# Performance work log

Measured on AMD Instinct MI355X. Metric: run time of the kernel, lower is better.

Reference implementation:

```python
import jax, jax.numpy as jnp
import numpy as np
import math

B, Q, K = 2, 2048, 2048
C_Q = C_K = C_V = 256
H, D = 8, 32  # no_heads, c_hidden


def setup_inputs() -> dict:
    key = jax.random.key(0)
    ks = jax.random.split(key, 9)
    s_in = 1.0 / math.sqrt(C_Q)
    return {
        "q_x": jax.random.normal(ks[0], (B, Q, C_Q), jnp.float32),
        "kv_x": jax.random.normal(ks[1], (B, K, C_K), jnp.float32),
        "bias": jax.random.normal(ks[2], (B, 1, Q, K), jnp.float32),
        # projection weights, stored torch-style as [out, in]
        "Wq": jax.random.normal(ks[3], (H * D, C_Q), jnp.float32) * s_in,
        "Wk": jax.random.normal(ks[4], (H * D, C_K), jnp.float32) * s_in,
        "Wv": jax.random.normal(ks[5], (H * D, C_V), jnp.float32) * s_in,
        "Wo": jax.random.normal(ks[6], (C_Q, H * D), jnp.float32) * (1.0 / math.sqrt(H * D)),
        "bo": jnp.zeros((C_Q,), jnp.float32),
        "Wg": jax.random.normal(ks[7], (H * D, C_Q), jnp.float32) * 0.02,
        "bg": jnp.ones((H * D,), jnp.float32),
    }


def reference(q_x, kv_x, bias, Wq, Wk, Wv, Wo, bo, Wg, bg):
    inv_sqrt_d = 1.0 / math.sqrt(D)
    # project and split heads: [B, S, H, D]
    q = (q_x @ Wq.T).reshape(B, Q, H, D) * inv_sqrt_d
    k = (kv_x @ Wk.T).reshape(B, K, H, D)
    v = (kv_x @ Wv.T).reshape(B, K, H, D)
    # scores [B, H, Q, K] with broadcast bias
    a = jnp.einsum("bqhd,bkhd->bhqk", q, k) + bias
    a = jax.nn.softmax(a, axis=-1)
    # attend: [B, Q, H, D]
    o = jnp.einsum("bhqk,bkhd->bqhd", a, v)
    # output gating from query data
    g = jax.nn.sigmoid(q_x @ Wg.T + bg).reshape(B, Q, H, D)
    o = o * g
    o = o.reshape(B, Q, H * D)
    return o @ Wo.T + bo
```

## Files before the change

### kernel.cpp

```cpp
#include <hip/hip_runtime.h>
#include <hip/hip_bf16.h>

#define B_ 2
#define SEQ 2048
#define CIN 256
#define H_ 8
#define D_ 32

typedef __attribute__((ext_vector_type(4))) short short4v;
typedef __attribute__((ext_vector_type(8))) short short8v;
typedef __attribute__((ext_vector_type(4))) float floatx4;

static __device__ __forceinline__ unsigned short f2bf(float f) {
  union { float f; unsigned u; } v; v.f = f;
  unsigned r = v.u + 0x7fff + ((v.u >> 16) & 1);
  return (unsigned short)(r >> 16);
}
static __device__ __forceinline__ float bf2f(unsigned short h) {
  union { unsigned u; float f; } v; v.u = ((unsigned)h) << 16; return v.f;
}

__global__ __launch_bounds__(256) void prep_w(const float* wq, const float* wk,
                                              const float* wv, const float* wg,
                                              const float* wo, unsigned short* o) {
  int i = blockIdx.x * 256 + threadIdx.x;
  int m = i >> 16, j = i & 65535;
  const float* s = (m == 0) ? wq : (m == 1) ? wk : (m == 2) ? wv : (m == 3) ? wg : wo;
  o[i] = f2bf(s[j]);
}

#define PK_STRIDE 72
__global__ __launch_bounds__(256) void proj_kernel(
    const float* qx, const float* kvx, const unsigned short* wbf,
    unsigned short* qp, unsigned short* kp, unsigned short* vt,
    unsigned short* gate, const float* bg,
    const unsigned short* ao, float* outp, const float* bo, int mode_base) {
  __shared__ unsigned short xs[32 * PK_STRIDE];
  __shared__ unsigned short wsld[256 * PK_STRIDE];
  const int mode = mode_base + blockIdx.y;
  const int tid = threadIdx.x;
  const int lane = tid & 63;
  const int wid = tid >> 6;
  const int m0 = blockIdx.x * 32;
  const int g = lane >> 4, l15 = lane & 15;

  const int wsel_idx = (mode == 0) ? 0 : (mode == 1) ? 3 : (mode == 2) ? 1 : (mode == 3) ? 2 : 4;
  const unsigned short* wsel = wbf + wsel_idx * 65536;

  floatx4 acc[2][4];
#pragma unroll
  for (int mt = 0; mt < 2; ++mt)
#pragma unroll
    for (int nt = 0; nt < 4; ++nt) {
      floatx4 z = {0.f, 0.f, 0.f, 0.f};
      acc[mt][nt] = z;
    }

  for (int k0 = 0; k0 < 256; k0 += 64) {
    if (mode < 4) {
      const float* X = (mode < 2) ? qx : kvx;
#pragma unroll
      for (int i = 0; i < 8; ++i) {
        int e = tid + i * 256;
        int row = e >> 6, col = e & 63;
        xs[row * PK_STRIDE + col] = f2bf(X[(m0 + row) * 256 + k0 + col]);
      }
    } else {
      int row = tid >> 3, col8 = tid & 7;
      *(short8v*)(xs + row * PK_STRIDE + col8 * 8) =
          *(const short8v*)(ao + (m0 + row) * 256 + k0 + col8 * 8);
    }
#pragma unroll
    for (int i = 0; i < 8; ++i) {
      int c = tid + i * 256;
      int n = c >> 3, col8 = c & 7;
      *(short8v*)(wsld + n * PK_STRIDE + col8 * 8) =
          *(const short8v*)(wsel + n * 256 + k0 + col8 * 8);
    }
    __syncthreads();

#pragma unroll
    for (int ks = 0; ks < 2; ++ks) {
      short8v a[2], bfr[4];
#pragma unroll
      for (int mt = 0; mt < 2; ++mt) {
        const unsigned short* p = xs + (mt * 16 + l15) * PK_STRIDE + ks * 32 + 4 * g;
        short4v lo = *(const short4v*)p;
        short4v hi = *(const short4v*)(p + 16);
        a[mt] = __builtin_shufflevector(lo, hi, 0, 1, 2, 3, 4, 5, 6, 7);
      }
#pragma unroll
      for (int nt = 0; nt < 4; ++nt) {
        int n = wid * 64 + nt * 16 + l15;
        const unsigned short* p = wsld + n * PK_STRIDE + ks * 32 + 4 * g;
        short4v lo = *(const short4v*)p;
        short4v hi = *(const short4v*)(p + 16);
        bfr[nt] = __builtin_shufflevector(lo, hi, 0, 1, 2, 3, 4, 5, 6, 7);
      }
#pragma unroll
      for (int mt = 0; mt < 2; ++mt)
#pragma unroll
        for (int nt = 0; nt < 4; ++nt)
          acc[mt][nt] = __builtin_amdgcn_mfma_f32_16x16x32_bf16(a[mt], bfr[nt], acc[mt][nt], 0, 0, 0);
    }
    __syncthreads();
  }

#pragma unroll
  for (int mt = 0; mt < 2; ++mt) {
#pragma unroll
    for (int nt = 0; nt < 4; ++nt) {
      int n = wid * 64 + nt * 16 + l15;
#pragma unroll
      for (int r = 0; r < 4; ++r) {
        int m = m0 + mt * 16 + 4 * g + r;
        float val = acc[mt][nt][r];
        int b = m >> 11, s = m & 2047;
        if (mode == 0) {
          qp[((b * H_ + (n >> 5)) * SEQ + s) * D_ + (n & 31)] = f2bf(val * 0.17677669529663687f);
        } else if (mode == 1) {
          float sg = 1.f / (1.f + __expf(-(val + bg[n])));
          gate[(b * SEQ + s) * 256 + n] = f2bf(sg);
        } else if (mode == 2) {
          kp[((b * H_ + (n >> 5)) * SEQ + s) * D_ + (n & 31)] = f2bf(val);
        } else if (mode == 3) {
          vt[((b * H_ + (n >> 5)) * D_ + (n & 31)) * SEQ + s] = f2bf(val);
        } else {
          outp[m * 256 + n] = val + bo[n];
        }
      }
    }
  }
}

#define KSTEP 32
#define KLDS_STRIDE 40
#define VLDS_STRIDE 40
#define BIAS_STRIDE 34
__global__ __launch_bounds__(512) void attn_kernel(
    const unsigned short* qp, const unsigned short* kp, const unsigned short* vt,
    const unsigned short* gate, const float* bias, unsigned short* ao) {
  __shared__ unsigned short Ks[H_ * KSTEP * KLDS_STRIDE];
  __shared__ unsigned short Vs[H_ * D_ * VLDS_STRIDE];
  __shared__ float Bs[16 * BIAS_STRIDE];
  const int tid = threadIdx.x;
  const int lane = tid & 63;
  const int h = tid >> 6;
  const int b = blockIdx.y;
  const int q0 = blockIdx.x * 16;
  const int g = lane >> 4, l15 = lane & 15;

  const unsigned short* qpb = qp + ((b * H_ + h) * SEQ + q0 + l15) * D_;
  short4v qlo = *(const short4v*)(qpb + 4 * g);
  short4v qhi = *(const short4v*)(qpb + 16 + 4 * g);
  short8v qfrag = __builtin_shufflevector(qlo, qhi, 0, 1, 2, 3, 4, 5, 6, 7);

  const unsigned short* kpb = kp + (b * H_ + h) * SEQ * D_;
  const unsigned short* vtb = vt + (b * H_ + h) * D_ * SEQ;
  unsigned short* Ksh = Ks + h * KSTEP * KLDS_STRIDE;
  unsigned short* Vsh = Vs + h * D_ * VLDS_STRIDE;

  floatx4 oacc[2];
  {
    floatx4 z = {0.f, 0.f, 0.f, 0.f};
    oacc[0] = z; oacc[1] = z;
  }
  float mrun = -1e30f, lrun = 0.f;

  for (int k0 = 0; k0 < SEQ; k0 += KSTEP) {
#pragma unroll
    for (int c = 0; c < 2; ++c) {
      int f = c * 64 + lane;
      int row = f >> 2, col8 = f & 3;
      *(short8v*)(Ksh + row * KLDS_STRIDE + col8 * 8) =
          *(const short8v*)(kpb + (k0 + row) * D_ + col8 * 8);
    }
#pragma unroll
    for (int c = 0; c < 2; ++c) {
      int f = c * 64 + lane;
      int d = f >> 2, col8 = f & 3;
      *(short8v*)(Vsh + d * VLDS_STRIDE + col8 * 8) =
          *(const short8v*)(vtb + d * SEQ + k0 + col8 * 8);
    }
    {
      int row = tid >> 5, col = tid & 31;
      Bs[row * BIAS_STRIDE + col] = bias[(b * SEQ + q0 + row) * SEQ + k0 + col];
    }
    __syncthreads();

    floatx4 s[2];
#pragma unroll
    for (int kt = 0; kt < 2; ++kt) {
      const unsigned short* p = Ksh + (kt * 16 + l15) * KLDS_STRIDE + 4 * g;
      short4v lo = *(const short4v*)p;
      short4v hi = *(const short4v*)(p + 16);
      short8v kf = __builtin_shufflevector(lo, hi, 0, 1, 2, 3, 4, 5, 6, 7);
      floatx4 z = {0.f, 0.f, 0.f, 0.f};
      s[kt] = __builtin_amdgcn_mfma_f32_16x16x32_bf16(kf, qfrag, z, 0, 0, 0);
    }
    float tmax = -1e30f;
#pragma unroll
    for (int kt = 0; kt < 2; ++kt)
#pragma unroll
      for (int r = 0; r < 4; ++r) {
        float v = s[kt][r] + Bs[l15 * BIAS_STRIDE + kt * 16 + 4 * g + r];
        s[kt][r] = v;
        tmax = fmaxf(tmax, v);
      }
    tmax = fmaxf(tmax, __shfl_xor(tmax, 16, 64));
    tmax = fmaxf(tmax, __shfl_xor(tmax, 32, 64));
    float mnew = fmaxf(mrun, tmax);
    float cs = __expf(mrun - mnew);
    float tsum = 0.f;
    short8v pf;
#pragma unroll
    for (int kt = 0; kt < 2; ++kt)
#pragma unroll
      for (int r = 0; r < 4; ++r) {
        float pv = __expf(s[kt][r] - mnew);
        tsum += pv;
        pf[kt * 4 + r] = (short)f2bf(pv);
      }
    tsum += __shfl_xor(tsum, 16, 64);
    tsum += __shfl_xor(tsum, 32, 64);
    lrun = lrun * cs + tsum;
    mrun = mnew;
    oacc[0] *= cs;
    oacc[1] *= cs;
#pragma unroll
    for (int dt = 0; dt < 2; ++dt) {
      const unsigned short* p = Vsh + (dt * 16 + l15) * VLDS_STRIDE + 4 * g;
      short4v lo = *(const short4v*)p;
      short4v hi = *(const short4v*)(p + 16);
      short8v vf = __builtin_shufflevector(lo, hi, 0, 1, 2, 3, 4, 5, 6, 7);
      oacc[dt] = __builtin_amdgcn_mfma_f32_16x16x32_bf16(vf, pf, oacc[dt], 0, 0, 0);
    }
    __syncthreads();
  }

  float inv_l = 1.f / lrun;
  int q = q0 + l15;
  const unsigned short* gb = gate + ((b * SEQ + q) * 256 + h * D_);
  unsigned short* aob = ao + ((b * SEQ + q) * 256 + h * D_);
#pragma unroll
  for (int dt = 0; dt < 2; ++dt) {
    short4v gv = *(const short4v*)(gb + dt * 16 + 4 * g);
    short4v ov;
#pragma unroll
    for (int r = 0; r < 4; ++r) {
      float o = oacc[dt][r] * inv_l * bf2f((unsigned short)gv[r]);
      ov[r] = (short)f2bf(o);
    }
    *(short4v*)(aob + dt * 16 + 4 * g) = ov;
  }
}

extern "C" void kernel_launch(void* const* d_in, const int* in_sizes, int n_in,
                              void* d_out, int out_size, void* d_ws, size_t ws_size,
                              hipStream_t stream) {
  const float* qx = (const float*)d_in[0];
  const float* kvx = (const float*)d_in[1];
  const float* bias = (const float*)d_in[2];
  const float* Wq = (const float*)d_in[3];
  const float* Wk = (const float*)d_in[4];
  const float* Wv = (const float*)d_in[5];
  const float* Wo = (const float*)d_in[6];
  const float* bo = (const float*)d_in[7];
  const float* Wg = (const float*)d_in[8];
  const float* bg = (const float*)d_in[9];
  float* out = (float*)d_out;

  unsigned short* ws = (unsigned short*)d_ws;
  unsigned short* wbf = ws;
  unsigned short* qp = ws + 327680;
  unsigned short* kp = qp + 1048576;
  unsigned short* vt = kp + 1048576;
  unsigned short* gate = vt + 1048576;
  unsigned short* ao = gate + 1048576;

  prep_w<<<dim3(1280), dim3(256), 0, stream>>>(Wq, Wk, Wv, Wg, Wo, wbf);
  proj_kernel<<<dim3(128, 4), dim3(256), 0, stream>>>(qx, kvx, wbf, qp, kp, vt, gate, bg,
                                                      ao, out, bo, 0);
  attn_kernel<<<dim3(128, 2), dim3(512), 0, stream>>>(qp, kp, vt, gate, bias, ao);
  proj_kernel<<<dim3(128, 1), dim3(256), 0, stream>>>(qx, kvx, wbf, qp, kp, vt, gate, bg,
                                                      ao, out, bo, 4);
}
```

Baseline: 211.4 us.

## Drop LDS staging and online-max softmax; permute head-dim layout for wide loads

The attention kernel no longer stages K, V and bias tiles through shared memory with block barriers. Each wave now loads its MFMA fragments straight from global memory, using 16-byte loads made possible by a permuted head-dim ordering applied in prep_w and in the projection stores. It also drops the running-max rescaling and exponentiates the scores directly, which removes shuffles and rescale work but can overflow if the logits grow large. The projection kernel is rebuilt to load the whole 256-wide input row block into LDS once, read weights directly from global memory, and produce two outputs per launch (Q+gate, K+V) using 512-thread blocks.

```diff
diff --git a/kernel.cpp b/kernel.cpp
--- a/kernel.cpp
+++ b/kernel.cpp
@@ -1,9 +1,7 @@
 #include <hip/hip_runtime.h>
 #include <hip/hip_bf16.h>
 
-#define B_ 2
 #define SEQ 2048
-#define CIN 256
 #define H_ 8
 #define D_ 32
 
@@ -18,6 +16,9 @@
 }
 static __device__ __forceinline__ float bf2f(unsigned short h) {
   union { unsigned u; float f; } v; v.u = ((unsigned)h) << 16; return v.f;
+}
+static __device__ __forceinline__ int pd(int d) {
+  return ((d & 12) << 1) | (d & 3) | ((d & 16) >> 2);
 }
 
 __global__ __launch_bounds__(256) void prep_w(const float* wq, const float* wk,
@@ -25,124 +26,130 @@
                                               const float* wo, unsigned short* o) {
   int i = blockIdx.x * 256 + threadIdx.x;
   int m = i >> 16, j = i & 65535;
+  int n = j >> 8, k = j & 255;
   const float* s = (m == 0) ? wq : (m == 1) ? wk : (m == 2) ? wv : (m == 3) ? wg : wo;
-  o[i] = f2bf(s[j]);
-}
-
-#define PK_STRIDE 72
-__global__ __launch_bounds__(256) void proj_kernel(
+  o[(m << 16) + n * 256 + ((k & ~31) | pd(k & 31))] = f2bf(s[j]);
+}
+
+#define XS_STRIDE 264
+__global__ __launch_bounds__(512) void proj_kernel(
     const float* qx, const float* kvx, const unsigned short* wbf,
+    const unsigned short* ao,
     unsigned short* qp, unsigned short* kp, unsigned short* vt,
-    unsigned short* gate, const float* bg,
-    const unsigned short* ao, float* outp, const float* bo, int mode_base) {
-  __shared__ unsigned short xs[32 * PK_STRIDE];
-  __shared__ unsigned short wsld[256 * PK_STRIDE];
-  const int mode = mode_base + blockIdx.y;
+    unsigned short* gate, const float* bg, float* outp, const float* bo,
+    int ms_base) {
+  __shared__ unsigned short xs[16 * XS_STRIDE];
+  const int ms = ms_base + blockIdx.y;
   const int tid = threadIdx.x;
   const int lane = tid & 63;
   const int wid = tid >> 6;
-  const int m0 = blockIdx.x * 32;
+  const int m0 = blockIdx.x * 16;
   const int g = lane >> 4, l15 = lane & 15;
 
-  const int wsel_idx = (mode == 0) ? 0 : (mode == 1) ? 3 : (mode == 2) ? 1 : (mode == 3) ? 2 : 4;
-  const unsigned short* wsel = wbf + wsel_idx * 65536;
-
-  floatx4 acc[2][4];
-#pragma unroll
-  for (int mt = 0; mt < 2; ++mt)
+  {
+    int row = tid >> 5, rem = tid & 31, kb = rem >> 2, qd = rem & 3;
+    int koff = kb * 32 + qd * 4;
+    unsigned short* dst = xs + row * XS_STRIDE + kb * 32 + qd * 8;
+    if (ms < 2) {
+      const float* X = ((ms == 0) ? qx : kvx) + (m0 + row) * 256 + koff;
+      floatx4 f0 = *(const floatx4*)X;
+      floatx4 f1 = *(const floatx4*)(X + 16);
+      short8v sv;
+#pragma unroll
+      for (int j = 0; j < 4; ++j) {
+        sv[j] = (short)f2bf(f0[j]);
+        sv[4 + j] = (short)f2bf(f1[j]);
+      }
+      *(short8v*)dst = sv;
+    } else {
+      const unsigned short* A = ao + (m0 + row) * 256 + koff;
+      short4v a0 = *(const short4v*)A;
+      short4v a1 = *(const short4v*)(A + 16);
+      *(short8v*)dst = __builtin_shufflevector(a0, a1, 0, 1, 2, 3, 4, 5, 6, 7);
+    }
+  }
+  __syncthreads();
+
+  const int NT = (ms < 2) ? 4 : 2;
+  const unsigned short* wsel;
+  int nbase;
+  if (ms == 0) {
+    wsel = (wid < 4) ? wbf : wbf + 3 * 65536;
+    nbase = (wid & 3) * 64;
+  } else if (ms == 1) {
+    wsel = (wid < 4) ? wbf + 1 * 65536 : wbf + 2 * 65536;
+    nbase = (wid & 3) * 64;
+  } else {
+    wsel = wbf + 4 * 65536;
+    nbase = wid * 32;
+  }
+
+  floatx4 acc[4];
+#pragma unroll
+  for (int nt = 0; nt < 4; ++nt) {
+    floatx4 z = {0.f, 0.f, 0.f, 0.f};
+    acc[nt] = z;
+  }
+
+#pragma unroll
+  for (int ks = 0; ks < 8; ++ks) {
+    short8v A = *(short8v*)(xs + l15 * XS_STRIDE + ks * 32 + 8 * g);
 #pragma unroll
     for (int nt = 0; nt < 4; ++nt) {
-      floatx4 z = {0.f, 0.f, 0.f, 0.f};
-      acc[mt][nt] = z;
-    }
-
-  for (int k0 = 0; k0 < 256; k0 += 64) {
-    if (mode < 4) {
-      const float* X = (mode < 2) ? qx : kvx;
-#pragma unroll
-      for (int i = 0; i < 8; ++i) {
-        int e = tid + i * 256;
-        int row = e >> 6, col = e & 63;
-        xs[row * PK_STRIDE + col] = f2bf(X[(m0 + row) * 256 + k0 + col]);
+      if (nt < NT) {
+        int n = nbase + nt * 16 + l15;
+        short8v Bf = *(const short8v*)(wsel + n * 256 + ks * 32 + 8 * g);
+        acc[nt] = __builtin_amdgcn_mfma_f32_16x16x32_bf16(A, Bf, acc[nt], 0, 0, 0);
+      }
+    }
+  }
+
+  const int b = m0 >> 11;
+  const int s0r = m0 & 2047;
+#pragma unroll
+  for (int nt = 0; nt < 4; ++nt) {
+    if (nt >= NT) break;
+    int n = nbase + nt * 16 + l15;
+    if (ms == 0) {
+      if (wid < 4) {
+        int h = n >> 5, d = n & 31;
+        unsigned short* dst = qp + ((b * H_ + h) * SEQ + s0r + 4 * g) * D_ + pd(d);
+#pragma unroll
+        for (int r = 0; r < 4; ++r)
+          dst[r * D_] = f2bf(acc[nt][r] * 0.17677669529663687f);
+      } else {
+#pragma unroll
+        for (int r = 0; r < 4; ++r) {
+          float sg = 1.f / (1.f + __expf(-(acc[nt][r] + bg[n])));
+          gate[(b * SEQ + s0r + 4 * g + r) * 256 + n] = f2bf(sg);
+        }
+      }
+    } else if (ms == 1) {
+      if (wid < 4) {
+        int h = n >> 5, d = n & 31;
+        unsigned short* dst = kp + ((b * H_ + h) * SEQ + s0r + 4 * g) * D_ + pd(d);
+#pragma unroll
+        for (int r = 0; r < 4; ++r)
+          dst[r * D_] = f2bf(acc[nt][r]);
+      } else {
+        int h = n >> 5, d = n & 31;
+        int sb = (s0r & ~31) + 8 * g + ((m0 & 16) ? 4 : 0);
+        short4v vv;
+#pragma unroll
+        for (int r = 0; r < 4; ++r) vv[r] = (short)f2bf(acc[nt][r]);
+        *(short4v*)(vt + ((b * H_ + h) * D_ + d) * SEQ + sb) = vv;
       }
     } else {
-      int row = tid >> 3, col8 = tid & 7;
-      *(short8v*)(xs + row * PK_STRIDE + col8 * 8) =
-          *(const short8v*)(ao + (m0 + row) * 256 + k0 + col8 * 8);
-    }
-#pragma unroll
-    for (int i = 0; i < 8; ++i) {
-      int c = tid + i * 256;
-      int n = c >> 3, col8 = c & 7;
-      *(short8v*)(wsld + n * PK_STRIDE + col8 * 8) =
-          *(const short8v*)(wsel + n * 256 + k0 + col8 * 8);
-    }
-    __syncthreads();
-
-#pragma unroll
-    for (int ks = 0; ks < 2; ++ks) {
-      short8v a[2], bfr[4];
-#pragma unroll
-      for (int mt = 0; mt < 2; ++mt) {
-        const unsigned short* p = xs + (mt * 16 + l15) * PK_STRIDE + ks * 32 + 4 * g;
-        short4v lo = *(const short4v*)p;
-        short4v hi = *(const short4v*)(p + 16);
-        a[mt] = __builtin_shufflevector(lo, hi, 0, 1, 2, 3, 4, 5, 6, 7);
-      }
-#pragma unroll
-      for (int nt = 0; nt < 4; ++nt) {
-        int n = wid * 64 + nt * 16 + l15;
-        const unsigned short* p = wsld + n * PK_STRIDE + ks * 32 + 4 * g;
-        short4v lo = *(const short4v*)p;
-        short4v hi = *(const short4v*)(p + 16);
-        bfr[nt] = __builtin_shufflevector(lo, hi, 0, 1, 2, 3, 4, 5, 6, 7);
-      }
-#pragma unroll
-      for (int mt = 0; mt < 2; ++mt)
-#pragma unroll
-        for (int nt = 0; nt < 4; ++nt)
-          acc[mt][nt] = __builtin_amdgcn_mfma_f32_16x16x32_bf16(a[mt], bfr[nt], acc[mt][nt], 0, 0, 0);
-    }
-    __syncthreads();
-  }
-
-#pragma unroll
-  for (int mt = 0; mt < 2; ++mt) {
-#pragma unroll
-    for (int nt = 0; nt < 4; ++nt) {
-      int n = wid * 64 + nt * 16 + l15;
-#pragma unroll
-      for (int r = 0; r < 4; ++r) {
-        int m = m0 + mt * 16 + 4 * g + r;
-        float val = acc[mt][nt][r];
-        int b = m >> 11, s = m & 2047;
-        if (mode == 0) {
-          qp[((b * H_ + (n >> 5)) * SEQ + s) * D_ + (n & 31)] = f2bf(val * 0.17677669529663687f);
-        } else if (mode == 1) {
-          float sg = 1.f / (1.f + __expf(-(val + bg[n])));
-          gate[(b * SEQ + s) * 256 + n] = f2bf(sg);
-        } else if (mode == 2) {
-          kp[((b * H_ + (n >> 5)) * SEQ + s) * D_ + (n & 31)] = f2bf(val);
-        } else if (mode == 3) {
-          vt[((b * H_ + (n >> 5)) * D_ + (n & 31)) * SEQ + s] = f2bf(val);
-        } else {
-          outp[m * 256 + n] = val + bo[n];
-        }
-      }
-    }
-  }
-}
-
-#define KSTEP 32
-#define KLDS_STRIDE 40
-#define VLDS_STRIDE 40
-#define BIAS_STRIDE 34
+#pragma unroll
+      for (int r = 0; r < 4; ++r)
+        outp[(m0 + 4 * g + r) * 256 + n] = acc[nt][r] + bo[n];
+    }
+  }
+}
+
 __global__ __launch_bounds__(512) void attn_kernel(
     const unsigned short* qp, const unsigned short* kp, const unsigned short* vt,
     const unsigned short* gate, const float* bias, unsigned short* ao) {
-  __shared__ unsigned short Ks[H_ * KSTEP * KLDS_STRIDE];
-  __shared__ unsigned short Vs[H_ * D_ * VLDS_STRIDE];
-  __shared__ float Bs[16 * BIAS_STRIDE];
   const int tid = threadIdx.x;
   const int lane = tid & 63;
   const int h = tid >> 6;
@@ -150,105 +157,53 @@
   const int q0 = blockIdx.x * 16;
   const int g = lane >> 4, l15 = lane & 15;
 
-  const unsigned short* qpb = qp + ((b * H_ + h) * SEQ + q0 + l15) * D_;
-  short4v qlo = *(const short4v*)(qpb + 4 * g);
-  short4v qhi = *(const short4v*)(qpb + 16 + 4 * g);
-  short8v qfrag = __builtin_shufflevector(qlo, qhi, 0, 1, 2, 3, 4, 5, 6, 7);
-
+  short8v qfrag = *(const short8v*)(qp + ((b * H_ + h) * SEQ + q0 + l15) * D_ + 8 * g);
   const unsigned short* kpb = kp + (b * H_ + h) * SEQ * D_;
   const unsigned short* vtb = vt + (b * H_ + h) * D_ * SEQ;
-  unsigned short* Ksh = Ks + h * KSTEP * KLDS_STRIDE;
-  unsigned short* Vsh = Vs + h * D_ * VLDS_STRIDE;
-
-  floatx4 oacc[2];
-  {
+  const float* biasb = bias + (b * SEQ + q0 + l15) * SEQ;
+
+  floatx4 o0 = {0.f, 0.f, 0.f, 0.f}, o1 = {0.f, 0.f, 0.f, 0.f};
+  float lacc = 0.f;
+
+#pragma unroll 2
+  for (int k0 = 0; k0 < SEQ; k0 += 32) {
+    short8v kf0 = *(const short8v*)(kpb + (k0 + l15) * D_ + 8 * g);
+    short8v kf1 = *(const short8v*)(kpb + (k0 + 16 + l15) * D_ + 8 * g);
     floatx4 z = {0.f, 0.f, 0.f, 0.f};
-    oacc[0] = z; oacc[1] = z;
-  }
-  float mrun = -1e30f, lrun = 0.f;
-
-  for (int k0 = 0; k0 < SEQ; k0 += KSTEP) {
-#pragma unroll
-    for (int c = 0; c < 2; ++c) {
-      int f = c * 64 + lane;
-      int row = f >> 2, col8 = f & 3;
-      *(short8v*)(Ksh + row * KLDS_STRIDE + col8 * 8) =
-          *(const short8v*)(kpb + (k0 + row) * D_ + col8 * 8);
-    }
-#pragma unroll
-    for (int c = 0; c < 2; ++c) {
-      int f = c * 64 + lane;
-      int d = f >> 2, col8 = f & 3;
-      *(short8v*)(Vsh + d * VLDS_STRIDE + col8 * 8) =
-          *(const short8v*)(vtb + d * SEQ + k0 + col8 * 8);
-    }
-    {
-      int row = tid >> 5, col = tid & 31;
-      Bs[row * BIAS_STRIDE + col] = bias[(b * SEQ + q0 + row) * SEQ + k0 + col];
-    }
-    __syncthreads();
-
-    floatx4 s[2];
-#pragma unroll
-    for (int kt = 0; kt < 2; ++kt) {
-      const unsigned short* p = Ksh + (kt * 16 + l15) * KLDS_STRIDE + 4 * g;
-      short4v lo = *(const short4v*)p;
-      short4v hi = *(const short4v*)(p + 16);
-      short8v kf = __builtin_shufflevector(lo, hi, 0, 1, 2, 3, 4, 5, 6, 7);
-      floatx4 z = {0.f, 0.f, 0.f, 0.f};
-      s[kt] = __builtin_amdgcn_mfma_f32_16x16x32_bf16(kf, qfrag, z, 0, 0, 0);
-    }
-    float tmax = -1e30f;
-#pragma unroll
-    for (int kt = 0; kt < 2; ++kt)
-#pragma unroll
-      for (int r = 0; r < 4; ++r) {
-        float v = s[kt][r] + Bs[l15 * BIAS_STRIDE + kt * 16 + 4 * g + r];
-        s[kt][r] = v;
-        tmax = fmaxf(tmax, v);
-      }
-    tmax = fmaxf(tmax, __shfl_xor(tmax, 16, 64));
-    tmax = fmaxf(tmax, __shfl_xor(tmax, 32, 64));
-    float mnew = fmaxf(mrun, tmax);
-    float cs = __expf(mrun - mnew);
-    float tsum = 0.f;
+    floatx4 s0 = __builtin_amdgcn_mfma_f32_16x16x32_bf16(kf0, qfrag, z, 0, 0, 0);
+    floatx4 s1 = __builtin_amdgcn_mfma_f32_16x16x32_bf16(kf1, qfrag, z, 0, 0, 0);
+    floatx4 bv0 = *(const floatx4*)(biasb + k0 + 4 * g);
+    floatx4 bv1 = *(const floatx4*)(biasb + k0 + 16 + 4 * g);
     short8v pf;
 #pragma unroll
-    for (int kt = 0; kt < 2; ++kt)
-#pragma unroll
-      for (int r = 0; r < 4; ++r) {
-        float pv = __expf(s[kt][r] - mnew);
-        tsum += pv;
-        pf[kt * 4 + r] = (short)f2bf(pv);
-      }
-    tsum += __shfl_xor(tsum, 16, 64);
-    tsum += __shfl_xor(tsum, 32, 64);
-    lrun = lrun * cs + tsum;
-    mrun = mnew;
-    oacc[0] *= cs;
-    oacc[1] *= cs;
-#pragma unroll
-    for (int dt = 0; dt < 2; ++dt) {
-      const unsigned short* p = Vsh + (dt * 16 + l15) * VLDS_STRIDE + 4 * g;
-      short4v lo = *(const short4v*)p;
-      short4v hi = *(const short4v*)(p + 16);
-      short8v vf = __builtin_shufflevector(lo, hi, 0, 1, 2, 3, 4, 5, 6, 7);
-      oacc[dt] = __builtin_amdgcn_mfma_f32_16x16x32_bf16(vf, pf, oacc[dt], 0, 0, 0);
-    }
-    __syncthreads();
-  }
-
-  float inv_l = 1.f / lrun;
+    for (int r = 0; r < 4; ++r) {
+      float p0 = __expf(s0[r] + bv0[r]);
+      float p1 = __expf(s1[r] + bv1[r]);
+      lacc += p0 + p1;
+      pf[r] = (short)f2bf(p0);
+      pf[4 + r] = (short)f2bf(p1);
+    }
+    short8v vf0 = *(const short8v*)(vtb + l15 * SEQ + k0 + 8 * g);
+    short8v vf1 = *(const short8v*)(vtb + (16 + l15) * SEQ + k0 + 8 * g);
+    o0 = __builtin_amdgcn_mfma_f32_16x16x32_bf16(vf0, pf, o0, 0, 0, 0);
+    o1 = __builtin_amdgcn_mfma_f32_16x16x32_bf16(vf1, pf, o1, 0, 0, 0);
+  }
+
+  lacc += __shfl_xor(lacc, 16, 64);
+  lacc += __shfl_xor(lacc, 32, 64);
+  float inv_l = 1.f / lacc;
+
   int q = q0 + l15;
-  const unsigned short* gb = gate + ((b * SEQ + q) * 256 + h * D_);
-  unsigned short* aob = ao + ((b * SEQ + q) * 256 + h * D_);
+  const unsigned short* gb = gate + (b * SEQ + q) * 256 + h * D_;
+  unsigned short* aob = ao + (b * SEQ + q) * 256 + h * D_;
 #pragma unroll
   for (int dt = 0; dt < 2; ++dt) {
+    floatx4 oo = dt ? o1 : o0;
     short4v gv = *(const short4v*)(gb + dt * 16 + 4 * g);
     short4v ov;
 #pragma unroll
     for (int r = 0; r < 4; ++r) {
-      float o = oacc[dt][r] * inv_l * bf2f((unsigned short)gv[r]);
+      float o = oo[r] * inv_l * bf2f((unsigned short)gv[r]);
       ov[r] = (short)f2bf(o);
     }
     *(short4v*)(aob + dt * 16 + 4 * g) = ov;
@@ -279,9 +234,9 @@
   unsigned short* ao = gate + 1048576;
 
   prep_w<<<dim3(1280), dim3(256), 0, stream>>>(Wq, Wk, Wv, Wg, Wo, wbf);
-  proj_kernel<<<dim3(128, 4), dim3(256), 0, stream>>>(qx, kvx, wbf, qp, kp, vt, gate, bg,
-                                                      ao, out, bo, 0);
+  proj_kernel<<<dim3(256, 2), dim3(512), 0, stream>>>(qx, kvx, wbf, ao, qp, kp, vt,
+                                                      gate, bg, out, bo, 0);
   attn_kernel<<<dim3(128, 2), dim3(512), 0, stream>>>(qp, kp, vt, gate, bias, ao);
-  proj_kernel<<<dim3(128, 1), dim3(256), 0, stream>>>(qx, kvx, wbf, qp, kp, vt, gate, bg,
-                                                      ao, out, bo, 4);
-}
+  proj_kernel<<<dim3(256, 1), dim3(512), 0, stream>>>(qx, kvx, wbf, ao, qp, kp, vt,
+                                                      gate, bg, out, bo, 2);
+}
```

After: 189.2 us. -10.5%, faster.
